# Kernel optimization log

Measured on AMD Instinct MI355X. Metric: run time of the kernel, lower is better.

The kernel has to match this reference:

```python
import jax, jax.numpy as jnp
import numpy as np

L, B, T, C, H, V = 8, 8, 1024, 768, 12, 1024
D = C // H  # head dim 64
FF = 4 * C
EPS = 1e-5


def _ln(h, g, b):
    mu = jnp.mean(h, axis=-1, keepdims=True)
    var = jnp.mean((h - mu) ** 2, axis=-1, keepdims=True)
    return (h - mu) * jax.lax.rsqrt(var + EPS) * g + b


def _ffn(h, W1, b1, W2, b2):
    return jax.nn.gelu(h @ W1 + b1, approximate=False) @ W2 + b2


def setup_inputs() -> dict:
    key = jax.random.key(0)
    ks = jax.random.split(key, 16)
    s = 0.02
    inp = {
        "x": jax.random.randint(ks[0], (B, T), 0, V),
        "embed": jax.random.normal(ks[1], (V, C), jnp.float32) * s,
        "pos": jax.random.normal(ks[2], (T, C), jnp.float32) * s,
        "Wqkv": jax.random.normal(ks[3], (L, C, 3 * C), jnp.float32) * s,
        "bqkv": jnp.zeros((L, 3 * C), jnp.float32),
        "W1a": jax.random.normal(ks[4], (L, C, FF), jnp.float32) * s,
        "b1a": jnp.zeros((L, FF), jnp.float32),
        "W2a": jax.random.normal(ks[5], (L, FF, C), jnp.float32) * s,
        "b2a": jnp.zeros((L, C), jnp.float32),
        "g1": jnp.ones((L, C), jnp.float32),
        "beta1": jnp.zeros((L, C), jnp.float32),
        "W1b": jax.random.normal(ks[6], (L, C, FF), jnp.float32) * s,
        "b1b": jnp.zeros((L, FF), jnp.float32),
        "W2b": jax.random.normal(ks[7], (L, FF, C), jnp.float32) * s,
        "b2b": jnp.zeros((L, C), jnp.float32),
        "g2": jnp.ones((L, C), jnp.float32),
        "beta2": jnp.zeros((L, C), jnp.float32),
        "lm_W": jax.random.normal(ks[8], (C, V), jnp.float32) * s,
        "lm_b": jnp.zeros((V,), jnp.float32),
    }
    return inp


def reference(x, embed, pos, Wqkv, bqkv, W1a, b1a, W2a, b2a, g1, beta1,
              W1b, b1b, W2b, b2b, g2, beta2, lm_W, lm_b):
    h = embed[x] + pos[:T]  # (B,T,C)
    causal = jnp.tril(jnp.ones((T, T), bool))

    def block(h, p):
        (Wqkv, bqkv, W1a, b1a, W2a, b2a, g1, beta1,
         W1b, b1b, W2b, b2b, g2, beta2) = p
        qkv = h @ Wqkv + bqkv  # (B,T,3C); split order is K,Q,V per source
        K, Q, Vv = jnp.split(qkv, 3, axis=-1)
        K = K.reshape(B, T, H, D).transpose(0, 2, 1, 3)
        Q = Q.reshape(B, T, H, D).transpose(0, 2, 1, 3)
        Vv = Vv.reshape(B, T, H, D).transpose(0, 2, 1, 3)
        att = jnp.einsum("bhqd,bhkd->bhqk", Q, K) / jnp.sqrt(jnp.float32(D))
        att = jnp.where(causal, att, -jnp.inf)
        att = jax.nn.softmax(att, axis=-1)
        y = jnp.einsum("bhqk,bhkd->bhqd", att, Vv)
        y = y.transpose(0, 2, 1, 3).reshape(B, T, C)
        y = _ffn(y, W1a, b1a, W2a, b2a)  # FFN inside SelfAttn
        h = h + _ln(y, g1, beta1)        # post-norm residual, as in source
        h = h + _ln(_ffn(h, W1b, b1b, W2b, b2b), g2, beta2)
        return h, None

    params = (Wqkv, bqkv, W1a, b1a, W2a, b2a, g1, beta1,
              W1b, b1b, W2b, b2b, g2, beta2)
    h, _ = jax.lax.scan(block, h, params)
    return h @ lm_W + lm_b  # (B,T,V) logits
```

## Files before the change

kernel.cpp:

```cpp
#include <hip/hip_runtime.h>
#include <hip/hip_bf16.h>

#define L_ 8
#define B_ 8
#define T_ 1024
#define C_ 768
#define H_ 12
#define D_HEAD 64
#define V_ 1024
#define FF_ 3072
#define M_ (B_ * T_)

typedef __bf16 bf16x8 __attribute__((ext_vector_type(8)));
typedef float f32x4 __attribute__((ext_vector_type(4)));

typedef const __attribute__((address_space(1))) void* as1cvp;
typedef __attribute__((address_space(3))) void* as3vp;

__device__ __forceinline__ void async16(const void* g, void* l) {
  __builtin_amdgcn_global_load_lds((as1cvp)g, (as3vp)l, 16, 0, 0);
}

__device__ __forceinline__ float bf2f(unsigned short u) {
  union { unsigned u32; float f; } c; c.u32 = ((unsigned)u) << 16; return c.f;
}

__device__ __forceinline__ unsigned short f2bf(float f) {
  __hip_bfloat16 h = __float2bfloat16(f);
  return *(unsigned short*)&h;
}

__device__ __forceinline__ float gelu_f(float x) {
  return 0.5f * x * (1.0f + erff(x * 0.70710678118654752f));
}

__global__ __launch_bounds__(256) void embed_kernel(
    const int* __restrict__ x, const float* __restrict__ emb,
    const float* __restrict__ pos, float* __restrict__ h,
    __hip_bfloat16* __restrict__ hb) {
  int row = blockIdx.x;
  int t = row & (T_ - 1);
  int id = x[row];
#pragma unroll
  for (int j = 0; j < 3; ++j) {
    int c = threadIdx.x + j * 256;
    float v = emb[(size_t)id * C_ + c] + pos[(size_t)t * C_ + c];
    h[(size_t)row * C_ + c] = v;
    hb[(size_t)row * C_ + c] = __float2bfloat16(v);
  }
}

__global__ void transpose_cast(const float* __restrict__ W,
                               __hip_bfloat16* __restrict__ Wt, int K, int N) {
  __shared__ float tile[32][33];
  int nb = blockIdx.x * 32, kb = blockIdx.y * 32;
  int tx = threadIdx.x, ty = threadIdx.y;
#pragma unroll
  for (int r = 0; r < 4; ++r)
    tile[ty + r * 8][tx] = W[(size_t)(kb + ty + r * 8) * N + nb + tx];
  __syncthreads();
#pragma unroll
  for (int r = 0; r < 4; ++r)
    Wt[(size_t)(nb + ty + r * 8) * K + kb + tx] =
        __float2bfloat16(tile[tx][ty + r * 8]);
}

__global__ void transpose_cast2(const float* __restrict__ Wa,
                                __hip_bfloat16* __restrict__ Wta,
                                const float* __restrict__ Wb,
                                __hip_bfloat16* __restrict__ Wtb, int K, int N) {
  __shared__ float tile[32][33];
  const float* W = blockIdx.z ? Wb : Wa;
  __hip_bfloat16* Wt = blockIdx.z ? Wtb : Wta;
  int nb = blockIdx.x * 32, kb = blockIdx.y * 32;
  int tx = threadIdx.x, ty = threadIdx.y;
#pragma unroll
  for (int r = 0; r < 4; ++r)
    tile[ty + r * 8][tx] = W[(size_t)(kb + ty + r * 8) * N + nb + tx];
  __syncthreads();
#pragma unroll
  for (int r = 0; r < 4; ++r)
    Wt[(size_t)(nb + ty + r * 8) * K + kb + tx] =
        __float2bfloat16(tile[tx][ty + r * 8]);
}

template <int ACT_GELU, int OUT_BF16>
__global__ __launch_bounds__(256, 2) void gemm_bt(
    const __hip_bfloat16* __restrict__ A, const __hip_bfloat16* __restrict__ Bt,
    const float* __restrict__ bias, void* __restrict__ Cv, int M, int N, int K) {
  __shared__ __align__(16) __hip_bfloat16 As[128 * 32];
  __shared__ __align__(16) __hip_bfloat16 Bs[128 * 32];
  const int tid = threadIdx.x;
  const int lane = tid & 63, wv = tid >> 6;
  const int lane4 = lane & 15, quad = lane >> 4;
  const int wr = wv >> 1, wc = wv & 1;
  const int bm = blockIdx.y * 128, bn = blockIdx.x * 128;

  const int r0 = tid >> 2, kc0 = (tid & 3) * 8;
  const __hip_bfloat16* gA0 = A + (size_t)(bm + r0) * K + kc0;
  const __hip_bfloat16* gA1 = gA0 + (size_t)64 * K;
  const __hip_bfloat16* gB0 = Bt + (size_t)(bn + r0) * K + kc0;
  const __hip_bfloat16* gB1 = gB0 + (size_t)64 * K;
  __hip_bfloat16* lA0 = As + tid * 8;
  __hip_bfloat16* lA1 = As + (tid + 256) * 8;
  __hip_bfloat16* lB0 = Bs + tid * 8;
  __hip_bfloat16* lB1 = Bs + (tid + 256) * 8;

  f32x4 acc[4][4] = {};

  for (int k0 = 0; k0 < K; k0 += 32) {
    async16(gA0 + k0, lA0);
    async16(gA1 + k0, lA1);
    async16(gB0 + k0, lB0);
    async16(gB1 + k0, lB1);
    __syncthreads();
    bf16x8 af[4], bfv[4];
#pragma unroll
    for (int i = 0; i < 4; ++i)
      af[i] = *(const bf16x8*)(As + (wr * 64 + i * 16 + lane4) * 32 + quad * 8);
#pragma unroll
    for (int j = 0; j < 4; ++j)
      bfv[j] = *(const bf16x8*)(Bs + (wc * 64 + j * 16 + lane4) * 32 + quad * 8);
#pragma unroll
    for (int i = 0; i < 4; ++i)
#pragma unroll
      for (int j = 0; j < 4; ++j)
        acc[i][j] = __builtin_amdgcn_mfma_f32_16x16x32_bf16(af[i], bfv[j],
                                                            acc[i][j], 0, 0, 0);
    __syncthreads();
  }

#pragma unroll
  for (int i = 0; i < 4; ++i) {
    int row0 = bm + wr * 64 + i * 16 + quad * 4;
#pragma unroll
    for (int j = 0; j < 4; ++j) {
      int col = bn + wc * 64 + j * 16 + lane4;
      float bv = bias[col];
#pragma unroll
      for (int r = 0; r < 4; ++r) {
        float v = acc[i][j][r] + bv;
        if (ACT_GELU) v = gelu_f(v);
        size_t off = (size_t)(row0 + r) * N + col;
        if (OUT_BF16)
          ((__hip_bfloat16*)Cv)[off] = __float2bfloat16(v);
        else
          ((float*)Cv)[off] = v;
      }
    }
  }
}

__global__ __launch_bounds__(256) void attn_mfma(
    const __hip_bfloat16* __restrict__ qkv, __hip_bfloat16* __restrict__ y) {
  __shared__ __align__(16) __hip_bfloat16 VtS[2][64][72];
  __shared__ __align__(16) __hip_bfloat16 Ps[2][4][16][72];

  const int tid = threadIdx.x;
  const int lane = tid & 63, w = tid >> 6;
  const int lane4 = lane & 15, quad = lane >> 4;
  const int bh = blockIdx.y;
  const int b = bh / H_, hh = bh % H_;
  const unsigned short* qk16 = (const unsigned short*)qkv;
  const size_t base = (size_t)b * T_ * (3 * C_) + hh * D_HEAD;
  const size_t tile_stride = (size_t)64 * (3 * C_);
  const int NTILE = T_ / 64;

  union FragU { bf16x8 v; unsigned short s[8]; uint4 q; };

  const unsigned short* kbase0 =
      qk16 + base + (size_t)lane4 * (3 * C_) + quad * 8;
  const unsigned short* vbase =
      qk16 + base + (size_t)lane * (3 * C_) + 2 * C_ + w * 16;

  int buf = 0;

  for (int qi = 0; qi < 2; ++qi) {
    const int qt = qi ? blockIdx.x : (NTILE - 1 - blockIdx.x);

    FragU aq[2];
    {
      const unsigned short* qp =
          qk16 + base + (size_t)(qt * 64 + w * 16 + lane4) * (3 * C_) + C_ +
          quad * 8;
#pragma unroll
      for (int c = 0; c < 2; ++c) {
        FragU t;
        t.q = *(const uint4*)(qp + c * 32);
#pragma unroll
        for (int j = 0; j < 8; ++j) aq[c].s[j] = f2bf(bf2f(t.s[j]) * 0.125f);
      }
    }

    f32x4 o_acc[4] = {};
    float m_r = -1e30f, l_r = 0.f;

    FragU kc[4][2];
    uint4 vc0, vc1;
    {
      const unsigned short* kp = kbase0;
#pragma unroll
      for (int nt = 0; nt < 4; ++nt) {
        kc[nt][0].q = *(const uint4*)(kp + nt * 16 * (3 * C_));
        kc[nt][1].q = *(const uint4*)(kp + nt * 16 * (3 * C_) + 32);
      }
      vc0 = *(const uint4*)vbase;
      vc1 = *(const uint4*)(vbase + 8);
    }

    for (int kt = 0; kt <= qt; ++kt) {
      FragU kn[4][2];
      uint4 vn0, vn1;
      {
        int ktn = (kt < qt) ? kt + 1 : qt;
        const unsigned short* kp = kbase0 + (size_t)ktn * tile_stride;
#pragma unroll
        for (int nt = 0; nt < 4; ++nt) {
          kn[nt][0].q = *(const uint4*)(kp + nt * 16 * (3 * C_));
          kn[nt][1].q = *(const uint4*)(kp + nt * 16 * (3 * C_) + 32);
        }
        const unsigned short* vp = vbase + (size_t)ktn * tile_stride;
        vn0 = *(const uint4*)vp;
        vn1 = *(const uint4*)(vp + 8);
      }

      f32x4 s_acc[4] = {};
#pragma unroll
      for (int nt = 0; nt < 4; ++nt) {
        s_acc[nt] = __builtin_amdgcn_mfma_f32_16x16x32_bf16(
            kc[nt][0].v, aq[0].v, s_acc[nt], 0, 0, 0);
        s_acc[nt] = __builtin_amdgcn_mfma_f32_16x16x32_bf16(
            kc[nt][1].v, aq[1].v, s_acc[nt], 0, 0, 0);
      }

      if (kt == qt) {
        int qloc = w * 16 + lane4;
#pragma unroll
        for (int nt = 0; nt < 4; ++nt) {
          int k0loc = nt * 16 + quad * 4;
#pragma unroll
          for (int r = 0; r < 4; ++r)
            if (k0loc + r > qloc) s_acc[nt][r] = -1e30f;
        }
      }

      float a0 = fmaxf(fmaxf(s_acc[0][0], s_acc[0][1]),
                       fmaxf(s_acc[0][2], s_acc[0][3]));
      float a1 = fmaxf(fmaxf(s_acc[1][0], s_acc[1][1]),
                       fmaxf(s_acc[1][2], s_acc[1][3]));
      float a2 = fmaxf(fmaxf(s_acc[2][0], s_acc[2][1]),
                       fmaxf(s_acc[2][2], s_acc[2][3]));
      float a3 = fmaxf(fmaxf(s_acc[3][0], s_acc[3][1]),
                       fmaxf(s_acc[3][2], s_acc[3][3]));
      float tm = fmaxf(fmaxf(a0, a1), fmaxf(a2, a3));
      tm = fmaxf(tm, __shfl_xor(tm, 16));
      tm = fmaxf(tm, __shfl_xor(tm, 32));
      float mn = fmaxf(m_r, tm);
      float alpha = __expf(m_r - mn);
      m_r = mn;

      float sr = 0.f;
#pragma unroll
      for (int nt = 0; nt < 4; ++nt) {
        float p0 = __expf(s_acc[nt][0] - mn);
        float p1 = __expf(s_acc[nt][1] - mn);
        float p2 = __expf(s_acc[nt][2] - mn);
        float p3 = __expf(s_acc[nt][3] - mn);
        sr += (p0 + p1) + (p2 + p3);
        union { unsigned short s[4]; uint2 u; } pk;
        pk.s[0] = f2bf(p0);
        pk.s[1] = f2bf(p1);
        pk.s[2] = f2bf(p2);
        pk.s[3] = f2bf(p3);
        *(uint2*)&Ps[buf][w][lane4][nt * 16 + quad * 4] = pk.u;
      }
      sr += __shfl_xor(sr, 16);
      sr += __shfl_xor(sr, 32);
      l_r = l_r * alpha + sr;

#pragma unroll
      for (int dt = 0; dt < 4; ++dt)
#pragma unroll
        for (int r = 0; r < 4; ++r) o_acc[dt][r] *= alpha;

      {
        const unsigned short* vs = (const unsigned short*)&vc0;
#pragma unroll
        for (int j = 0; j < 8; ++j)
          *(unsigned short*)&VtS[buf][w * 16 + j][lane] = vs[j];
        vs = (const unsigned short*)&vc1;
#pragma unroll
        for (int j = 0; j < 8; ++j)
          *(unsigned short*)&VtS[buf][w * 16 + 8 + j][lane] = vs[j];
      }

      __syncthreads();

      FragU pp0, pp1;
      pp0.v = *(const bf16x8*)&Ps[buf][w][lane4][quad * 8];
      pp1.v = *(const bf16x8*)&Ps[buf][w][lane4][32 + quad * 8];
#pragma unroll
      for (int dt = 0; dt < 4; ++dt) {
        bf16x8 bv0 = *(const bf16x8*)&VtS[buf][dt * 16 + lane4][quad * 8];
        bf16x8 bv1 = *(const bf16x8*)&VtS[buf][dt * 16 + lane4][32 + quad * 8];
        o_acc[dt] = __builtin_amdgcn_mfma_f32_16x16x32_bf16(bv0, pp0.v,
                                                            o_acc[dt], 0, 0, 0);
        o_acc[dt] = __builtin_amdgcn_mfma_f32_16x16x32_bf16(bv1, pp1.v,
                                                            o_acc[dt], 0, 0, 0);
      }

#pragma unroll
      for (int nt = 0; nt < 4; ++nt) {
        kc[nt][0] = kn[nt][0];
        kc[nt][1] = kn[nt][1];
      }
      vc0 = vn0;
      vc1 = vn1;
      buf ^= 1;
    }

    float invl = 1.f / l_r;
    int qrow = qt * 64 + w * 16 + lane4;
    unsigned short* yp =
        (unsigned short*)y + (size_t)(b * T_ + qrow) * C_ + hh * D_HEAD;
#pragma unroll
    for (int dt = 0; dt < 4; ++dt) {
      union { unsigned short s[4]; uint2 u; } ok;
#pragma unroll
      for (int r = 0; r < 4; ++r) ok.s[r] = f2bf(o_acc[dt][r] * invl);
      *(uint2*)(yp + dt * 16 + quad * 4) = ok.u;
    }
  }
}

__global__ __launch_bounds__(256) void resid_ln(
    float* __restrict__ h, const float* __restrict__ z,
    const float* __restrict__ g, const float* __restrict__ be,
    __hip_bfloat16* __restrict__ hb) {
  int row = blockIdx.x;
  int tid = threadIdx.x;
  const float* zr = z + (size_t)row * C_;
  float v[3], s = 0.f, s2 = 0.f;
#pragma unroll
  for (int j = 0; j < 3; ++j) {
    v[j] = zr[tid + 256 * j];
    s += v[j];
    s2 += v[j] * v[j];
  }
#pragma unroll
  for (int msk = 1; msk < 64; msk <<= 1) {
    s += __shfl_xor(s, msk);
    s2 += __shfl_xor(s2, msk);
  }
  __shared__ float red[8];
  int w = tid >> 6;
  if ((tid & 63) == 0) { red[w] = s; red[4 + w] = s2; }
  __syncthreads();
  s = red[0] + red[1] + red[2] + red[3];
  s2 = red[4] + red[5] + red[6] + red[7];
  float mu = s * (1.f / C_);
  float var = s2 * (1.f / C_) - mu * mu;
  float rstd = rsqrtf(var + 1e-5f);
  float* hr = h + (size_t)row * C_;
  __hip_bfloat16* hbr = hb + (size_t)row * C_;
#pragma unroll
  for (int j = 0; j < 3; ++j) {
    int c = tid + 256 * j;
    float nv = hr[c] + (v[j] - mu) * rstd * g[c] + be[c];
    hr[c] = nv;
    hbr[c] = __float2bfloat16(nv);
  }
}

extern "C" void kernel_launch(void* const* d_in, const int* in_sizes, int n_in,
                              void* d_out, int out_size, void* d_ws,
                              size_t ws_size, hipStream_t stream) {
  const int* x = (const int*)d_in[0];
  const float* embed = (const float*)d_in[1];
  const float* pos = (const float*)d_in[2];
  const float* Wqkv = (const float*)d_in[3];
  const float* bqkv = (const float*)d_in[4];
  const float* W1a = (const float*)d_in[5];
  const float* b1a = (const float*)d_in[6];
  const float* W2a = (const float*)d_in[7];
  const float* b2a = (const float*)d_in[8];
  const float* g1 = (const float*)d_in[9];
  const float* be1 = (const float*)d_in[10];
  const float* W1b = (const float*)d_in[11];
  const float* b1b = (const float*)d_in[12];
  const float* W2b = (const float*)d_in[13];
  const float* b2b = (const float*)d_in[14];
  const float* g2 = (const float*)d_in[15];
  const float* be2 = (const float*)d_in[16];
  const float* lmW = (const float*)d_in[17];
  const float* lmb = (const float*)d_in[18];
  float* out = (float*)d_out;

  char* p = (char*)d_ws;
  auto alloc = [&](size_t bytes) {
    void* r = (void*)p;
    p += (bytes + 255) & ~(size_t)255;
    return r;
  };
  float* h = (float*)alloc((size_t)M_ * C_ * 4);
  __hip_bfloat16* hb = (__hip_bfloat16*)alloc((size_t)M_ * C_ * 2);
  __hip_bfloat16* qkv = (__hip_bfloat16*)alloc((size_t)M_ * 3 * C_ * 2);
  __hip_bfloat16* ybuf = (__hip_bfloat16*)alloc((size_t)M_ * C_ * 2);
  __hip_bfloat16* ubuf = (__hip_bfloat16*)alloc((size_t)M_ * FF_ * 2);
  float* zbuf = (float*)alloc((size_t)M_ * C_ * 4);
  __hip_bfloat16* Wtqkv = (__hip_bfloat16*)alloc((size_t)(3 * C_) * C_ * 2);
  __hip_bfloat16* Wt1a = (__hip_bfloat16*)alloc((size_t)FF_ * C_ * 2);
  __hip_bfloat16* Wt1b = (__hip_bfloat16*)alloc((size_t)FF_ * C_ * 2);
  __hip_bfloat16* Wt2a = (__hip_bfloat16*)alloc((size_t)C_ * FF_ * 2);
  __hip_bfloat16* Wt2b = (__hip_bfloat16*)alloc((size_t)C_ * FF_ * 2);

  dim3 blk256(256);
  embed_kernel<<<M_, blk256, 0, stream>>>(x, embed, pos, h, hb);

  for (int l = 0; l < L_; ++l) {
    transpose_cast<<<dim3(3 * C_ / 32, C_ / 32), dim3(32, 8), 0, stream>>>(
        Wqkv + (size_t)l * C_ * 3 * C_, Wtqkv, C_, 3 * C_);
    transpose_cast2<<<dim3(FF_ / 32, C_ / 32, 2), dim3(32, 8), 0, stream>>>(
        W1a + (size_t)l * C_ * FF_, Wt1a, W1b + (size_t)l * C_ * FF_, Wt1b,
        C_, FF_);
    transpose_cast2<<<dim3(C_ / 32, FF_ / 32, 2), dim3(32, 8), 0, stream>>>(
        W2a + (size_t)l * FF_ * C_, Wt2a, W2b + (size_t)l * FF_ * C_, Wt2b,
        FF_, C_);

    gemm_bt<0, 1><<<dim3(3 * C_ / 128, M_ / 128), blk256, 0, stream>>>(
        hb, Wtqkv, bqkv + (size_t)l * 3 * C_, qkv, M_, 3 * C_, C_);
    attn_mfma<<<dim3(T_ / 128, B_ * H_), blk256, 0, stream>>>(qkv, ybuf);
    gemm_bt<1, 1><<<dim3(FF_ / 128, M_ / 128), blk256, 0, stream>>>(
        ybuf, Wt1a, b1a + (size_t)l * FF_, ubuf, M_, FF_, C_);
    gemm_bt<0, 0><<<dim3(C_ / 128, M_ / 128), blk256, 0, stream>>>(
        ubuf, Wt2a, b2a + (size_t)l * C_, zbuf, M_, C_, FF_);
    resid_ln<<<M_, blk256, 0, stream>>>(h, zbuf, g1 + (size_t)l * C_,
                                        be1 + (size_t)l * C_, hb);
    gemm_bt<1, 1><<<dim3(FF_ / 128, M_ / 128), blk256, 0, stream>>>(
        hb, Wt1b, b1b + (size_t)l * FF_, ubuf, M_, FF_, C_);
    gemm_bt<0, 0><<<dim3(C_ / 128, M_ / 128), blk256, 0, stream>>>(
        ubuf, Wt2b, b2b + (size_t)l * C_, zbuf, M_, C_, FF_);
    resid_ln<<<M_, blk256, 0, stream>>>(h, zbuf, g2 + (size_t)l * C_,
                                        be2 + (size_t)l * C_, hb);
  }

  transpose_cast<<<dim3(V_ / 32, C_ / 32), dim3(32, 8), 0, stream>>>(
      lmW, Wtqkv, C_, V_);
  gemm_bt<0, 0><<<dim3(V_ / 128, M_ / 128), blk256, 0, stream>>>(
      hb, Wtqkv, lmb, out, M_, V_, C_);
}
```

Before: 3.733 ms.

## Double-buffer GEMM LDS tiles and split-K the FF down-projections

Measured after the change: 3.686 ms. About the same (-1.3%).

```diff
diff --git a/kernel.cpp b/kernel.cpp
--- a/kernel.cpp
+++ b/kernel.cpp
@@ -87,40 +87,50 @@
 template <int ACT_GELU, int OUT_BF16>
 __global__ __launch_bounds__(256, 2) void gemm_bt(
     const __hip_bfloat16* __restrict__ A, const __hip_bfloat16* __restrict__ Bt,
-    const float* __restrict__ bias, void* __restrict__ Cv, int M, int N, int K) {
-  __shared__ __align__(16) __hip_bfloat16 As[128 * 32];
-  __shared__ __align__(16) __hip_bfloat16 Bs[128 * 32];
+    const float* __restrict__ bias, void* __restrict__ Cv,
+    float* __restrict__ C2, int M, int N, int K) {
+  __shared__ __align__(16) __hip_bfloat16 As[2][128 * 32];
+  __shared__ __align__(16) __hip_bfloat16 Bs[2][128 * 32];
   const int tid = threadIdx.x;
   const int lane = tid & 63, wv = tid >> 6;
   const int lane4 = lane & 15, quad = lane >> 4;
   const int wr = wv >> 1, wc = wv & 1;
   const int bm = blockIdx.y * 128, bn = blockIdx.x * 128;
 
+  const int kz = blockIdx.z;
+  const int Ksub = K / gridDim.z;
+
   const int r0 = tid >> 2, kc0 = (tid & 3) * 8;
-  const __hip_bfloat16* gA0 = A + (size_t)(bm + r0) * K + kc0;
+  const __hip_bfloat16* gA0 = A + (size_t)(bm + r0) * K + kz * Ksub + kc0;
   const __hip_bfloat16* gA1 = gA0 + (size_t)64 * K;
-  const __hip_bfloat16* gB0 = Bt + (size_t)(bn + r0) * K + kc0;
+  const __hip_bfloat16* gB0 = Bt + (size_t)(bn + r0) * K + kz * Ksub + kc0;
   const __hip_bfloat16* gB1 = gB0 + (size_t)64 * K;
-  __hip_bfloat16* lA0 = As + tid * 8;
-  __hip_bfloat16* lA1 = As + (tid + 256) * 8;
-  __hip_bfloat16* lB0 = Bs + tid * 8;
-  __hip_bfloat16* lB1 = Bs + (tid + 256) * 8;
+
+  auto stage = [&](int bsel, int k0) {
+    async16(gA0 + k0, As[bsel] + tid * 8);
+    async16(gA1 + k0, As[bsel] + (tid + 256) * 8);
+    async16(gB0 + k0, Bs[bsel] + tid * 8);
+    async16(gB1 + k0, Bs[bsel] + (tid + 256) * 8);
+  };
 
   f32x4 acc[4][4] = {};
 
-  for (int k0 = 0; k0 < K; k0 += 32) {
-    async16(gA0 + k0, lA0);
-    async16(gA1 + k0, lA1);
-    async16(gB0 + k0, lB0);
-    async16(gB1 + k0, lB1);
-    __syncthreads();
+  stage(0, 0);
+  __syncthreads();
+
+  const int nsteps = Ksub / 32;
+  for (int s = 0; s < nsteps; ++s) {
+    const int cur = s & 1;
+    if (s + 1 < nsteps) stage(cur ^ 1, (s + 1) * 32);
     bf16x8 af[4], bfv[4];
 #pragma unroll
     for (int i = 0; i < 4; ++i)
-      af[i] = *(const bf16x8*)(As + (wr * 64 + i * 16 + lane4) * 32 + quad * 8);
+      af[i] =
+          *(const bf16x8*)(As[cur] + (wr * 64 + i * 16 + lane4) * 32 + quad * 8);
 #pragma unroll
     for (int j = 0; j < 4; ++j)
-      bfv[j] = *(const bf16x8*)(Bs + (wc * 64 + j * 16 + lane4) * 32 + quad * 8);
+      bfv[j] =
+          *(const bf16x8*)(Bs[cur] + (wc * 64 + j * 16 + lane4) * 32 + quad * 8);
 #pragma unroll
     for (int i = 0; i < 4; ++i)
 #pragma unroll
@@ -130,13 +140,14 @@
     __syncthreads();
   }
 
+  float* outf = (kz == 0) ? (float*)Cv : C2;
 #pragma unroll
   for (int i = 0; i < 4; ++i) {
     int row0 = bm + wr * 64 + i * 16 + quad * 4;
 #pragma unroll
     for (int j = 0; j < 4; ++j) {
       int col = bn + wc * 64 + j * 16 + lane4;
-      float bv = bias[col];
+      float bv = (kz == 0) ? bias[col] : 0.f;
 #pragma unroll
       for (int r = 0; r < 4; ++r) {
         float v = acc[i][j][r] + bv;
@@ -145,7 +156,7 @@
         if (OUT_BF16)
           ((__hip_bfloat16*)Cv)[off] = __float2bfloat16(v);
         else
-          ((float*)Cv)[off] = v;
+          outf[off] = v;
       }
     }
   }
@@ -333,17 +344,19 @@
   }
 }
 
-__global__ __launch_bounds__(256) void resid_ln(
-    float* __restrict__ h, const float* __restrict__ z,
-    const float* __restrict__ g, const float* __restrict__ be,
-    __hip_bfloat16* __restrict__ hb) {
+__global__ __launch_bounds__(256) void resid_ln2(
+    float* __restrict__ h, const float* __restrict__ z0,
+    const float* __restrict__ z1, const float* __restrict__ g,
+    const float* __restrict__ be, __hip_bfloat16* __restrict__ hb) {
   int row = blockIdx.x;
   int tid = threadIdx.x;
-  const float* zr = z + (size_t)row * C_;
+  const float* zr0 = z0 + (size_t)row * C_;
+  const float* zr1 = z1 + (size_t)row * C_;
   float v[3], s = 0.f, s2 = 0.f;
 #pragma unroll
   for (int j = 0; j < 3; ++j) {
-    v[j] = zr[tid + 256 * j];
+    int c = tid + 256 * j;
+    v[j] = zr0[c] + zr1[c];
     s += v[j];
     s2 += v[j] * v[j];
   }
@@ -413,6 +426,7 @@
   __hip_bfloat16* Wt1b = (__hip_bfloat16*)alloc((size_t)FF_ * C_ * 2);
   __hip_bfloat16* Wt2a = (__hip_bfloat16*)alloc((size_t)C_ * FF_ * 2);
   __hip_bfloat16* Wt2b = (__hip_bfloat16*)alloc((size_t)C_ * FF_ * 2);
+  float* zpart = (float*)qkv;
 
   dim3 blk256(256);
   embed_kernel<<<M_, blk256, 0, stream>>>(x, embed, pos, h, hb);
@@ -428,24 +442,24 @@
         FF_, C_);
 
     gemm_bt<0, 1><<<dim3(3 * C_ / 128, M_ / 128), blk256, 0, stream>>>(
-        hb, Wtqkv, bqkv + (size_t)l * 3 * C_, qkv, M_, 3 * C_, C_);
+        hb, Wtqkv, bqkv + (size_t)l * 3 * C_, qkv, nullptr, M_, 3 * C_, C_);
     attn_mfma<<<dim3(T_ / 128, B_ * H_), blk256, 0, stream>>>(qkv, ybuf);
     gemm_bt<1, 1><<<dim3(FF_ / 128, M_ / 128), blk256, 0, stream>>>(
-        ybuf, Wt1a, b1a + (size_t)l * FF_, ubuf, M_, FF_, C_);
-    gemm_bt<0, 0><<<dim3(C_ / 128, M_ / 128), blk256, 0, stream>>>(
-        ubuf, Wt2a, b2a + (size_t)l * C_, zbuf, M_, C_, FF_);
-    resid_ln<<<M_, blk256, 0, stream>>>(h, zbuf, g1 + (size_t)l * C_,
-                                        be1 + (size_t)l * C_, hb);
+        ybuf, Wt1a, b1a + (size_t)l * FF_, ubuf, nullptr, M_, FF_, C_);
+    gemm_bt<0, 0><<<dim3(C_ / 128, M_ / 128, 2), blk256, 0, stream>>>(
+        ubuf, Wt2a, b2a + (size_t)l * C_, zbuf, zpart, M_, C_, FF_);
+    resid_ln2<<<M_, blk256, 0, stream>>>(h, zbuf, zpart, g1 + (size_t)l * C_,
+                                         be1 + (size_t)l * C_, hb);
     gemm_bt<1, 1><<<dim3(FF_ / 128, M_ / 128), blk256, 0, stream>>>(
-        hb, Wt1b, b1b + (size_t)l * FF_, ubuf, M_, FF_, C_);
-    gemm_bt<0, 0><<<dim3(C_ / 128, M_ / 128), blk256, 0, stream>>>(
-        ubuf, Wt2b, b2b + (size_t)l * C_, zbuf, M_, C_, FF_);
-    resid_ln<<<M_, blk256, 0, stream>>>(h, zbuf, g2 + (size_t)l * C_,
-                                        be2 + (size_t)l * C_, hb);
+        hb, Wt1b, b1b + (size_t)l * FF_, ubuf, nullptr, M_, FF_, C_);
+    gemm_bt<0, 0><<<dim3(C_ / 128, M_ / 128, 2), blk256, 0, stream>>>(
+        ubuf, Wt2b, b2b + (size_t)l * C_, zbuf, zpart, M_, C_, FF_);
+    resid_ln2<<<M_, blk256, 0, stream>>>(h, zbuf, zpart, g2 + (size_t)l * C_,
+                                         be2 + (size_t)l * C_, hb);
   }
 
   transpose_cast<<<dim3(V_ / 32, C_ / 32), dim3(32, 8), 0, stream>>>(
       lmW, Wtqkv, C_, V_);
   gemm_bt<0, 0><<<dim3(V_ / 128, M_ / 128), blk256, 0, stream>>>(
-      hb, Wtqkv, lmb, out, M_, V_, C_);
-}
+      hb, Wtqkv, lmb, out, nullptr, M_, V_, C_);
+}
```
